# Optimization experiments

Hardware: AMD Instinct MI355X
Metric: run time of the kernel (lower is better)

The kernel has to match this reference:

```python
import jax, jax.numpy as jnp
import numpy as np

N_HEAD = 8
HEAD_DIM = 128
WINDOW = 512
ROPE_BASE = 10000.0


def _rope_tables(T, dtype):
    # inv_freq: [head_dim/2]
    inv_freq = 1.0 / (ROPE_BASE ** (jnp.arange(0, HEAD_DIM, 2, dtype=jnp.float32) / HEAD_DIM))
    t = jnp.arange(T, dtype=jnp.float32)
    freqs = jnp.einsum('i,j->ij', t, inv_freq)          # [T, head_dim/2]
    emb = jnp.concatenate([freqs, freqs], axis=-1)       # [T, head_dim]
    return jnp.cos(emb).astype(dtype), jnp.sin(emb).astype(dtype)


def _rotate_half(x):
    d = x.shape[-1] // 2
    return jnp.concatenate([-x[..., d:], x[..., :d]], axis=-1)


def setup_inputs() -> dict:
    key = jax.random.key(0)
    k1, k2, k3 = jax.random.split(key, 3)
    B, T, C = 2, 4096, 1024
    x = jax.random.normal(k1, (B, T, C), dtype=jnp.float32)
    w_qkv = jax.random.normal(k2, (3 * C, C), dtype=jnp.float32) * (1.0 / np.sqrt(C))
    w_o = jax.random.normal(k3, (C, C), dtype=jnp.float32) * (1.0 / np.sqrt(C))
    return {"x": x, "w_qkv": w_qkv, "w_o": w_o}


def reference(x, w_qkv, w_o):
    B, T, C = x.shape
    scale = 1.0 / np.sqrt(HEAD_DIM)
    qkv = x @ w_qkv.T                                     # [B,T,3C]
    q, k, v = jnp.split(qkv, 3, axis=-1)
    # [B, H, T, D]
    q = q.reshape(B, T, N_HEAD, HEAD_DIM).transpose(0, 2, 1, 3)
    k = k.reshape(B, T, N_HEAD, HEAD_DIM).transpose(0, 2, 1, 3)
    v = v.reshape(B, T, N_HEAD, HEAD_DIM).transpose(0, 2, 1, 3)
    cos, sin = _rope_tables(T, x.dtype)                   # [T, D]
    cos = cos[None, None]
    sin = sin[None, None]
    q = q * cos + _rotate_half(q) * sin
    k = k * cos + _rotate_half(k) * sin
    attn = jnp.einsum('bhqd,bhkd->bhqk', q, k) * scale    # [B,H,T,T]
    i = jnp.arange(T)[:, None]
    j = jnp.arange(T)[None, :]
    # causal (j<=i) AND sliding window triu(diag=-W) (j >= i - W)
    keep = (j <= i) & (j >= i - WINDOW)
    neg = jnp.finfo(attn.dtype).min
    attn = jnp.where(keep[None, None], attn, neg)
    attn = jax.nn.softmax(attn, axis=-1)
    out = jnp.einsum('bhqk,bhkd->bhqd', attn, v)          # [B,H,T,D]
    out = out.transpose(0, 2, 1, 3).reshape(B, T, C)
    return out @ w_o.T
```

## Files before the change

kernel.cpp:

```cpp
#include <hip/hip_runtime.h>
#include <hip/hip_bf16.h>

typedef unsigned short us;
typedef __attribute__((ext_vector_type(8))) __bf16 bf16x8;
typedef __attribute__((ext_vector_type(4))) float f32x4;

#define MFMA16(a, b, c) __builtin_amdgcn_mfma_f32_16x16x32_bf16(a, b, c, 0, 0, 0)

static __device__ __forceinline__ us f2bf(float f) {
  __hip_bfloat16 h = __float2bfloat16(f);
  return __builtin_bit_cast(us, h);
}

static __device__ __forceinline__ void gll16(const us* g, us* l) {
  __builtin_amdgcn_global_load_lds((const __attribute__((address_space(1))) void*)g,
                                   (__attribute__((address_space(3))) void*)l,
                                   16, 0, 0);
}

__global__ void prep_kernel(const float* __restrict__ x, const float* __restrict__ wq,
                            const float* __restrict__ wo, us* __restrict__ xb,
                            us* __restrict__ wqb, us* __restrict__ wob,
                            float* __restrict__ ct, float* __restrict__ st) {
  const int blk = blockIdx.x;
  const int tid = threadIdx.x;
  if (blk < 12288) {
    const float* in;
    us* out;
    int i;
    if (blk < 8192)      { in = x;  out = xb;  i = blk * 256 + tid; }
    else if (blk < 11264){ in = wq; out = wqb; i = (blk - 8192) * 256 + tid; }
    else                 { in = wo; out = wob; i = (blk - 11264) * 256 + tid; }
    float4 v = ((const float4*)in)[i];
    ushort4 o;
    o.x = f2bf(v.x); o.y = f2bf(v.y); o.z = f2bf(v.z); o.w = f2bf(v.w);
    ((ushort4*)out)[i] = o;
  } else {
    int i = (blk - 12288) * 256 + tid;
    int t = i >> 6, d = i & 63;
    float ang = (float)t * exp2f((float)d * -0.20762050593046014f);
    float s, c;
    sincosf(ang, &s, &c);
    ct[i] = c;
    st[i] = s;
  }
}

__global__ __launch_bounds__(256, 2)
void qkv_rope_kernel(const us* __restrict__ A, const us* __restrict__ B,
                     const float* __restrict__ ctab, const float* __restrict__ stab,
                     us* __restrict__ qb, us* __restrict__ kb, us* __restrict__ vtb) {
  __shared__ __align__(16) char smem_raw[128 * 132 * 4];
  us* sA = (us*)smem_raw;
  us* sB = sA + 128 * 64;
  float* sC = (float*)smem_raw;
  us* sCus = (us*)smem_raw;

  const int tid = threadIdx.x;
  const int lane = tid & 63;
  const int wave = tid >> 6;
  const int l15 = lane & 15;
  const int lq = lane >> 4;
  const int m0 = blockIdx.x * 128;
  const int n0 = blockIdx.y * 128;
  const int wm = (wave & 1) * 64;
  const int wn2 = (wave >> 1) * 32;

  f32x4 acc[4][4] = {};

  for (int k0 = 0; k0 < 1024; k0 += 64) {
    for (int i = 0; i < 4; ++i) {
      int c = wave * 4 + i;
      int P = c * 64 + lane;
      int row = P >> 3;
      int cb = (P & 7) ^ (row & 7);
      gll16(A + (size_t)(m0 + row) * 1024 + k0 + cb * 8, sA + c * 512);
      gll16(B + (size_t)(n0 + row) * 1024 + k0 + cb * 8, sB + c * 512);
    }
    __syncthreads();
#pragma unroll
    for (int kk = 0; kk < 64; kk += 32) {
      const int cbr = (kk + lq * 8) >> 3;
      bf16x8 av[4], bv[4];
#pragma unroll
      for (int mt = 0; mt < 4; ++mt) {
        int m = wm + mt * 16 + l15;
        av[mt] = *(const bf16x8*)(sA + (m * 8 + (cbr ^ (m & 7))) * 8);
      }
#pragma unroll
      for (int nt = 0; nt < 4; ++nt) {
        int n = wn2 + (nt & 1) * 16 + (nt >> 1) * 64 + l15;
        bv[nt] = *(const bf16x8*)(sB + (n * 8 + (cbr ^ (n & 7))) * 8);
      }
#pragma unroll
      for (int mt = 0; mt < 4; ++mt)
#pragma unroll
        for (int nt = 0; nt < 4; ++nt)
          acc[mt][nt] = MFMA16(av[mt], bv[nt], acc[mt][nt]);
    }
    __syncthreads();
  }

  const int b = m0 >> 12;
  const int t0 = m0 & 4095;
  const int which = blockIdx.y >> 3;
  const int h = blockIdx.y & 7;

  if (which < 2) {
    us* outp = (which == 0) ? qb : kb;
    const size_t obase = ((size_t)(b * 8 + h)) * 4096 * 128;
#pragma unroll
    for (int mt = 0; mt < 4; ++mt)
#pragma unroll
      for (int r = 0; r < 4; ++r) {
        const int row = wm + mt * 16 + lq * 4 + r;
        const int tg = t0 + row;
        const float* cp = ctab + tg * 64 + wn2 + l15;
        const float* sp = stab + tg * 64 + wn2 + l15;
        const float c0 = cp[0], c1 = cp[16], s0 = sp[0], s1 = sp[16];
#pragma unroll
        for (int nt = 0; nt < 4; ++nt) {
          float xv = acc[mt][nt][r];
          float xp = acc[mt][nt ^ 2][r];
          float rot = (nt < 2) ? -xp : xp;
          float y = xv * ((nt & 1) ? c1 : c0) + rot * ((nt & 1) ? s1 : s0);
          sCus[row * 136 + wn2 + (nt & 1) * 16 + (nt >> 1) * 64 + l15] = f2bf(y);
        }
      }
    __syncthreads();
    for (int r = 0; r < 8; ++r) {
      int row = (tid >> 4) + r * 16;
      int col = (tid & 15) * 8;
      uint4 v = *(const uint4*)(sCus + row * 136 + col);
      *(uint4*)(outp + obase + (size_t)(t0 + row) * 128 + col) = v;
    }
  } else {
#pragma unroll
    for (int mt = 0; mt < 4; ++mt)
#pragma unroll
      for (int nt = 0; nt < 4; ++nt) {
        const int col = wn2 + (nt & 1) * 16 + (nt >> 1) * 64 + l15;
#pragma unroll
        for (int r = 0; r < 4; ++r)
          sC[(wm + mt * 16 + lq * 4 + r) * 129 + col] = acc[mt][nt][r];
      }
    __syncthreads();
    for (int r = 0; r < 8; ++r) {
      int d = (tid >> 4) + r * 16;
      int tl0 = (tid & 15) * 8;
      union { us u[8]; uint4 v; } tmp;
#pragma unroll
      for (int j = 0; j < 8; ++j)
        tmp.u[j] = f2bf(sC[(tl0 + j) * 129 + d]);
      *(uint4*)(vtb + ((size_t)((b * 8 + h) * 128 + d)) * 4096 + t0 + tl0) = tmp.v;
    }
  }
}

template <int MASK>
__device__ __forceinline__ void p_write(f32x4 (&s)[2][4], us* __restrict__ sP,
                                        int t0, int tj0, int wm2, int lq, int l15) {
  const float C2 = 0.08838834764831845f * 1.4426950408889634f;
#pragma unroll
  for (int mt = 0; mt < 2; ++mt)
#pragma unroll
    for (int nt = 0; nt < 4; ++nt) {
      const int jg = tj0 + nt * 16 + l15;
      const int cb = (nt * 16 + l15) >> 3;
      const int co = l15 & 7;
#pragma unroll
      for (int r = 0; r < 4; ++r) {
        const int rowl = wm2 + mt * 16 + lq * 4 + r;
        float v = s[mt][nt][r];
        if (MASK == 1) v = (jg + 512 >= t0 + rowl) ? v : -3.0e38f;
        if (MASK == 2) v = (jg <= t0 + rowl) ? v : -3.0e38f;
        sP[rowl * 64 + ((cb ^ (rowl & 7)) * 8) + co] = f2bf(exp2f(v * C2));
      }
    }
}

__global__ __launch_bounds__(256, 2)
void flash_kernel(const us* __restrict__ qg, const us* __restrict__ kg,
                  const us* __restrict__ vg, us* __restrict__ ao) {
  __shared__ us smem[40960];
  us* sK = smem;
  us* sV = smem + 16384;
  us* sP = smem + 32768;

  const int tid = threadIdx.x;
  const int lane = tid & 63;
  const int wave = tid >> 6;
  const int l15 = lane & 15;
  const int lq = lane >> 4;
  const int qx = blockIdx.x;
  const int h = blockIdx.y;
  const int b = blockIdx.z;
  const int t0 = qx * 128;
  const size_t bh = (size_t)(b * 8 + h);
  const int wm2 = wave * 32;

  bf16x8 qf[2][4];
#pragma unroll
  for (int mt = 0; mt < 2; ++mt)
#pragma unroll
    for (int ks = 0; ks < 4; ++ks)
      qf[mt][ks] = *(const bf16x8*)(qg + (bh * 4096 + t0 + wm2 + mt * 16 + l15) * 128 +
                                    ks * 32 + lq * 8);

  union { us u[8]; bf16x8 v; } one_u;
#pragma unroll
  for (int i = 0; i < 8; ++i) one_u.u[i] = 0x3F80;
  const bf16x8 vone = one_u.v;

  f32x4 o[2][9] = {};

  const int lo = t0 - 512;
  const int jtmin = (lo <= 0) ? 0 : (lo >> 6);
  const int jtmax = (t0 + 127) >> 6;
  const bool wmask = (t0 >= 512);

  auto stage = [&](int jt, int buf) {
    const int tj0 = jt * 64;
    us* dK = sK + buf * 8192;
    us* dV = sV + buf * 8192;
    for (int i = 0; i < 4; ++i) {
      int c = wave * 4 + i;
      int P = c * 64 + lane;
      int rowK = P >> 4;
      int cbK = (P & 15) ^ (rowK & 15);
      gll16(kg + (bh * 4096 + tj0 + rowK) * 128 + cbK * 8, dK + c * 512);
      int rowV = P >> 3;
      int cbV = (P & 7) ^ (rowV & 7);
      gll16(vg + (bh * 128 + rowV) * 4096 + tj0 + cbV * 8, dV + c * 512);
    }
  };

  stage(jtmin, 0);
  int cur = 0;

  for (int jt = jtmin; jt <= jtmax; ++jt) {
    __syncthreads();
    if (jt < jtmax) stage(jt + 1, cur ^ 1);

    const int tj0 = jt * 64;
    const us* sKc = sK + cur * 8192;
    const us* sVc = sV + cur * 8192;

    f32x4 s[2][4] = {};
#pragma unroll
    for (int ks = 0; ks < 4; ++ks) {
      const int cbr = ks * 4 + lq;
#pragma unroll
      for (int nt = 0; nt < 4; ++nt) {
        int n = nt * 16 + l15;
        bf16x8 bk = *(const bf16x8*)(sKc + (n * 16 + (cbr ^ (n & 15))) * 8);
#pragma unroll
        for (int mt = 0; mt < 2; ++mt)
          s[mt][nt] = MFMA16(qf[mt][ks], bk, s[mt][nt]);
      }
    }

    if (jt >= jtmax - 1)               p_write<2>(s, sP, t0, tj0, wm2, lq, l15);
    else if (wmask && jt <= jtmin + 1) p_write<1>(s, sP, t0, tj0, wm2, lq, l15);
    else                               p_write<0>(s, sP, t0, tj0, wm2, lq, l15);

#pragma unroll
    for (int ks = 0; ks < 2; ++ks) {
#pragma unroll
      for (int mt = 0; mt < 2; ++mt) {
        bf16x8 ap = *(const bf16x8*)(sP + (wm2 + mt * 16 + l15) * 64 +
                                     (((ks * 4 + lq) ^ (l15 & 7)) * 8));
#pragma unroll
        for (int dt = 0; dt < 8; ++dt) {
          int dd = dt * 16 + l15;
          bf16x8 bv = *(const bf16x8*)(sVc + (dd * 8 + ((ks * 4 + lq) ^ (dd & 7))) * 8);
          o[mt][dt] = MFMA16(ap, bv, o[mt][dt]);
        }
        o[mt][8] = MFMA16(ap, vone, o[mt][8]);
      }
    }
    cur ^= 1;
  }

#pragma unroll
  for (int mt = 0; mt < 2; ++mt)
#pragma unroll
    for (int r = 0; r < 4; ++r) {
      const float inv = 1.0f / o[mt][8][r];
      const int rowl = wm2 + mt * 16 + lq * 4 + r;
      const size_t base = ((size_t)b * 4096 + t0 + rowl) * 1024 + h * 128;
#pragma unroll
      for (int dt = 0; dt < 8; ++dt)
        ao[base + dt * 16 + l15] = f2bf(o[mt][dt][r] * inv);
    }
}

__global__ __launch_bounds__(256, 2)
void out_proj_kernel(const us* __restrict__ A, const us* __restrict__ B, float* __restrict__ C) {
  __shared__ us sA[128 * 64];
  __shared__ us sB[128 * 64];
  const int tid = threadIdx.x;
  const int lane = tid & 63;
  const int wave = tid >> 6;
  const int l15 = lane & 15;
  const int lq = lane >> 4;
  const int m0 = blockIdx.x * 128;
  const int n0 = blockIdx.y * 128;
  const int wm = (wave & 1) * 64;
  const int wn = (wave >> 1) * 64;
  f32x4 acc[4][4] = {};
  for (int k0 = 0; k0 < 1024; k0 += 64) {
    for (int i = 0; i < 4; ++i) {
      int c = wave * 4 + i;
      int P = c * 64 + lane;
      int row = P >> 3;
      int cb = (P & 7) ^ (row & 7);
      gll16(A + (size_t)(m0 + row) * 1024 + k0 + cb * 8, sA + c * 512);
      gll16(B + (size_t)(n0 + row) * 1024 + k0 + cb * 8, sB + c * 512);
    }
    __syncthreads();
#pragma unroll
    for (int kk = 0; kk < 64; kk += 32) {
      const int cbr = (kk + lq * 8) >> 3;
      bf16x8 av[4], bv[4];
#pragma unroll
      for (int mt = 0; mt < 4; ++mt) {
        int m = wm + mt * 16 + l15;
        av[mt] = *(const bf16x8*)(sA + (m * 8 + (cbr ^ (m & 7))) * 8);
      }
#pragma unroll
      for (int nt = 0; nt < 4; ++nt) {
        int n = wn + nt * 16 + l15;
        bv[nt] = *(const bf16x8*)(sB + (n * 8 + (cbr ^ (n & 7))) * 8);
      }
#pragma unroll
      for (int mt = 0; mt < 4; ++mt)
#pragma unroll
        for (int nt = 0; nt < 4; ++nt)
          acc[mt][nt] = MFMA16(av[mt], bv[nt], acc[mt][nt]);
    }
    __syncthreads();
  }
#pragma unroll
  for (int mt = 0; mt < 4; ++mt)
#pragma unroll
    for (int nt = 0; nt < 4; ++nt)
#pragma unroll
      for (int r = 0; r < 4; ++r)
        C[(size_t)(m0 + wm + mt * 16 + lq * 4 + r) * 1024 + (n0 + wn + nt * 16 + l15)] =
            acc[mt][nt][r];
}

extern "C" void kernel_launch(void* const* d_in, const int* in_sizes, int n_in,
                              void* d_out, int out_size, void* d_ws, size_t ws_size,
                              hipStream_t stream) {
  const float* x     = (const float*)d_in[0];
  const float* w_qkv = (const float*)d_in[1];
  const float* w_o   = (const float*)d_in[2];
  float* out = (float*)d_out;

  us* xb  = (us*)d_ws;
  us* wqb = xb  + (size_t)8192 * 1024;
  us* wob = wqb + (size_t)3072 * 1024;
  us* qb  = wob + (size_t)1024 * 1024;
  us* kb  = qb  + (size_t)2 * 8 * 4096 * 128;
  us* vtb = kb  + (size_t)2 * 8 * 4096 * 128;
  us* aob = vtb + (size_t)2 * 8 * 4096 * 128;
  float* ctab = (float*)(aob + (size_t)8192 * 1024);
  float* stab = ctab + (size_t)4096 * 64;

  prep_kernel<<<13312, 256, 0, stream>>>(x, w_qkv, w_o, xb, wqb, wob, ctab, stab);
  qkv_rope_kernel<<<dim3(64, 24), 256, 0, stream>>>(xb, wqb, ctab, stab, qb, kb, vtb);
  flash_kernel<<<dim3(32, 8, 2), 256, 0, stream>>>(qb, kb, vtb, aob);
  out_proj_kernel<<<dim3(64, 8), 256, 0, stream>>>(aob, wob, out);
}
```

Measured before the change: 208.2 us.

## Rewrite QKV GEMM as 256x256 tile, 8-wave double-buffered pipelined kernel

The QKV projection GEMM moves from 128x128 tiles with 4 waves to 256x256 tiles with 8 waves. LDS is double-buffered and each K-step is split into four quarter phases that interleave LDS fragment reads, asynchronous global-to-LDS prefetch of the next tiles, and MFMA bursts. Raised wave priority and explicit waitcnt and barriers are used to overlap loads with compute. The epilogue now handles two heads per block, with RoPE and the V transpose going through LDS. This gives more reuse per loaded byte and fewer blocks (384), at the cost of more registers, a complex schedule, and possible tail imbalance across CUs.

```diff
diff --git a/kernel.cpp b/kernel.cpp
--- a/kernel.cpp
+++ b/kernel.cpp
@@ -6,6 +6,7 @@
 typedef __attribute__((ext_vector_type(4))) float f32x4;
 
 #define MFMA16(a, b, c) __builtin_amdgcn_mfma_f32_16x16x32_bf16(a, b, c, 0, 0, 0)
+#define FENCE asm volatile("" ::: "memory")
 
 static __device__ __forceinline__ us f2bf(float f) {
   __hip_bfloat16 h = __float2bfloat16(f);
@@ -46,113 +47,210 @@
   }
 }
 
-__global__ __launch_bounds__(256, 2)
+__global__ __launch_bounds__(512, 2)
 void qkv_rope_kernel(const us* __restrict__ A, const us* __restrict__ B,
                      const float* __restrict__ ctab, const float* __restrict__ stab,
                      us* __restrict__ qb, us* __restrict__ kb, us* __restrict__ vtb) {
-  __shared__ __align__(16) char smem_raw[128 * 132 * 4];
-  us* sA = (us*)smem_raw;
-  us* sB = sA + 128 * 64;
-  float* sC = (float*)smem_raw;
-  us* sCus = (us*)smem_raw;
+  __shared__ __align__(16) us smem[65536];
+  us* sAb = smem;
+  us* sBb = smem + 32768;
 
   const int tid = threadIdx.x;
   const int lane = tid & 63;
   const int wave = tid >> 6;
   const int l15 = lane & 15;
   const int lq = lane >> 4;
-  const int m0 = blockIdx.x * 128;
-  const int n0 = blockIdx.y * 128;
-  const int wm = (wave & 1) * 64;
-  const int wn2 = (wave >> 1) * 32;
-
-  f32x4 acc[4][4] = {};
-
-  for (int k0 = 0; k0 < 1024; k0 += 64) {
-    for (int i = 0; i < 4; ++i) {
-      int c = wave * 4 + i;
-      int P = c * 64 + lane;
-      int row = P >> 3;
-      int cb = (P & 7) ^ (row & 7);
-      gll16(A + (size_t)(m0 + row) * 1024 + k0 + cb * 8, sA + c * 512);
-      gll16(B + (size_t)(n0 + row) * 1024 + k0 + cb * 8, sB + c * 512);
-    }
-    __syncthreads();
-#pragma unroll
-    for (int kk = 0; kk < 64; kk += 32) {
-      const int cbr = (kk + lq * 8) >> 3;
-      bf16x8 av[4], bv[4];
-#pragma unroll
-      for (int mt = 0; mt < 4; ++mt) {
-        int m = wm + mt * 16 + l15;
-        av[mt] = *(const bf16x8*)(sA + (m * 8 + (cbr ^ (m & 7))) * 8);
-      }
-#pragma unroll
-      for (int nt = 0; nt < 4; ++nt) {
-        int n = wn2 + (nt & 1) * 16 + (nt >> 1) * 64 + l15;
-        bv[nt] = *(const bf16x8*)(sB + (n * 8 + (cbr ^ (n & 7))) * 8);
-      }
-#pragma unroll
-      for (int mt = 0; mt < 4; ++mt)
-#pragma unroll
-        for (int nt = 0; nt < 4; ++nt)
-          acc[mt][nt] = MFMA16(av[mt], bv[nt], acc[mt][nt]);
-    }
-    __syncthreads();
+  const int wr = wave >> 2;
+  const int wc = wave & 3;
+  const int m0 = blockIdx.x * 256;
+  const int n0 = blockIdx.y * 256;
+
+  auto stage = [&](const us* gbase, us* lds, int j) {
+    int P = j * 512 + tid;
+    int row = P >> 3;
+    int sb = (P & 7) ^ (row & 7);
+    gll16(gbase + (size_t)row * 1024 + sb * 8, lds + (j * 512 + wave * 64) * 8);
+  };
+  auto stage_half = [&](int t, int h) {
+    int c = t & 1;
+    const us* g;
+    us* l;
+    if (h < 2) { g = A + (size_t)(m0 + h * 128) * 1024 + t * 64; l = sAb + c * 16384 + h * 8192; }
+    else       { g = B + (size_t)(n0 + (h - 2) * 128) * 1024 + t * 64; l = sBb + c * 16384 + (h - 2) * 8192; }
+    stage(g, l, 0);
+    stage(g, l, 1);
+  };
+  auto nrow = [&](int nt) {
+    return (wc >> 1) * 128 + (wc & 1) * 32 + (nt & 1) * 16 + (nt >> 1) * 64 + l15;
+  };
+
+  f32x4 acc[8][4] = {};
+  bf16x8 a0[4][2], a1[4][2], b0[2][2], b1[2][2];
+
+#pragma unroll
+  for (int h = 0; h < 4; ++h) stage_half(0, h);
+  stage_half(1, 0); stage_half(1, 1); stage_half(1, 2);
+  asm volatile("s_waitcnt vmcnt(6)" ::: "memory");
+  FENCE; __builtin_amdgcn_s_barrier(); FENCE;
+
+  for (int kt = 0; kt < 16; ++kt) {
+    const int c = kt & 1;
+    const us* sAc = sAb + c * 16384;
+    const us* sBc = sBb + c * 16384;
+
+#pragma unroll
+    for (int mt = 0; mt < 4; ++mt)
+#pragma unroll
+      for (int kk = 0; kk < 2; ++kk) {
+        int m = wr * 128 + mt * 16 + l15;
+        a0[mt][kk] = *(const bf16x8*)(sAc + m * 64 + (((kk * 4 + lq) ^ (m & 7)) * 8));
+      }
+#pragma unroll
+    for (int nt = 0; nt < 2; ++nt)
+#pragma unroll
+      for (int kk = 0; kk < 2; ++kk) {
+        int n = nrow(nt);
+        b0[nt][kk] = *(const bf16x8*)(sBc + n * 64 + (((kk * 4 + lq) ^ (n & 7)) * 8));
+      }
+    if (kt < 15) stage_half(kt + 1, 3);
+    FENCE; __builtin_amdgcn_s_barrier(); FENCE;
+    asm volatile("s_waitcnt lgkmcnt(0)" ::: "memory");
+    __builtin_amdgcn_sched_barrier(0);
+    __builtin_amdgcn_s_setprio(1);
+#pragma unroll
+    for (int mt = 0; mt < 4; ++mt)
+#pragma unroll
+      for (int nt = 0; nt < 2; ++nt)
+#pragma unroll
+        for (int kk = 0; kk < 2; ++kk)
+          acc[mt][nt] = MFMA16(a0[mt][kk], b0[nt][kk], acc[mt][nt]);
+    __builtin_amdgcn_s_setprio(0);
+    FENCE; __builtin_amdgcn_s_barrier(); FENCE;
+
+#pragma unroll
+    for (int mt = 0; mt < 4; ++mt)
+#pragma unroll
+      for (int kk = 0; kk < 2; ++kk) {
+        int m = wr * 128 + 64 + mt * 16 + l15;
+        a1[mt][kk] = *(const bf16x8*)(sAc + m * 64 + (((kk * 4 + lq) ^ (m & 7)) * 8));
+      }
+    FENCE; __builtin_amdgcn_s_barrier(); FENCE;
+    asm volatile("s_waitcnt lgkmcnt(0)" ::: "memory");
+    __builtin_amdgcn_sched_barrier(0);
+    __builtin_amdgcn_s_setprio(1);
+#pragma unroll
+    for (int mt = 0; mt < 4; ++mt)
+#pragma unroll
+      for (int nt = 0; nt < 2; ++nt)
+#pragma unroll
+        for (int kk = 0; kk < 2; ++kk)
+          acc[4 + mt][nt] = MFMA16(a1[mt][kk], b0[nt][kk], acc[4 + mt][nt]);
+    __builtin_amdgcn_s_setprio(0);
+    FENCE; __builtin_amdgcn_s_barrier(); FENCE;
+
+#pragma unroll
+    for (int nt = 0; nt < 2; ++nt)
+#pragma unroll
+      for (int kk = 0; kk < 2; ++kk) {
+        int n = nrow(2 + nt);
+        b1[nt][kk] = *(const bf16x8*)(sBc + n * 64 + (((kk * 4 + lq) ^ (n & 7)) * 8));
+      }
+    if (kt < 14) stage_half(kt + 2, 0);
+    FENCE; __builtin_amdgcn_s_barrier(); FENCE;
+    asm volatile("s_waitcnt lgkmcnt(0)" ::: "memory");
+    __builtin_amdgcn_sched_barrier(0);
+    __builtin_amdgcn_s_setprio(1);
+#pragma unroll
+    for (int mt = 0; mt < 4; ++mt)
+#pragma unroll
+      for (int nt = 0; nt < 2; ++nt)
+#pragma unroll
+        for (int kk = 0; kk < 2; ++kk)
+          acc[4 + mt][2 + nt] = MFMA16(a1[mt][kk], b1[nt][kk], acc[4 + mt][2 + nt]);
+    __builtin_amdgcn_s_setprio(0);
+    FENCE; __builtin_amdgcn_s_barrier(); FENCE;
+
+    if (kt < 14) { stage_half(kt + 2, 1); stage_half(kt + 2, 2); }
+    FENCE; __builtin_amdgcn_s_barrier(); FENCE;
+    __builtin_amdgcn_s_setprio(1);
+#pragma unroll
+    for (int mt = 0; mt < 4; ++mt)
+#pragma unroll
+      for (int nt = 0; nt < 2; ++nt)
+#pragma unroll
+        for (int kk = 0; kk < 2; ++kk)
+          acc[mt][2 + nt] = MFMA16(a0[mt][kk], b1[nt][kk], acc[mt][2 + nt]);
+    __builtin_amdgcn_s_setprio(0);
+    if (kt < 14) { asm volatile("s_waitcnt vmcnt(6)" ::: "memory"); }
+    else         { asm volatile("s_waitcnt vmcnt(0)" ::: "memory"); }
+    FENCE; __builtin_amdgcn_s_barrier(); FENCE;
   }
 
   const int b = m0 >> 12;
-  const int t0 = m0 & 4095;
-  const int which = blockIdx.y >> 3;
-  const int h = blockIdx.y & 7;
+  const int tg0 = m0 & 4095;
+  const int g0 = blockIdx.y * 2;
+  const int which = g0 >> 3;
+  us* sE = smem;
 
   if (which < 2) {
     us* outp = (which == 0) ? qb : kb;
-    const size_t obase = ((size_t)(b * 8 + h)) * 4096 * 128;
-#pragma unroll
-    for (int mt = 0; mt < 4; ++mt)
-#pragma unroll
-      for (int r = 0; r < 4; ++r) {
-        const int row = wm + mt * 16 + lq * 4 + r;
-        const int tg = t0 + row;
-        const float* cp = ctab + tg * 64 + wn2 + l15;
-        const float* sp = stab + tg * 64 + wn2 + l15;
-        const float c0 = cp[0], c1 = cp[16], s0 = sp[0], s1 = sp[16];
-#pragma unroll
-        for (int nt = 0; nt < 4; ++nt) {
-          float xv = acc[mt][nt][r];
-          float xp = acc[mt][nt ^ 2][r];
-          float rot = (nt < 2) ? -xp : xp;
-          float y = xv * ((nt & 1) ? c1 : c0) + rot * ((nt & 1) ? s1 : s0);
-          sCus[row * 136 + wn2 + (nt & 1) * 16 + (nt >> 1) * 64 + l15] = f2bf(y);
-        }
-      }
-    __syncthreads();
-    for (int r = 0; r < 8; ++r) {
-      int row = (tid >> 4) + r * 16;
-      int col = (tid & 15) * 8;
-      uint4 v = *(const uint4*)(sCus + row * 136 + col);
-      *(uint4*)(outp + obase + (size_t)(t0 + row) * 128 + col) = v;
+    for (int ch = 0; ch < 2; ++ch) {
+      const int h = (g0 + ch) & 7;
+      if ((wc >> 1) == ch) {
+        const int dl0 = (wc & 1) * 32 + l15;
+#pragma unroll
+        for (int mt = 0; mt < 8; ++mt)
+#pragma unroll
+          for (int r = 0; r < 4; ++r) {
+            const int row = wr * 128 + mt * 16 + lq * 4 + r;
+            const int tg = tg0 + row;
+            const float c0 = ctab[tg * 64 + dl0], c1 = ctab[tg * 64 + dl0 + 16];
+            const float s0 = stab[tg * 64 + dl0], s1 = stab[tg * 64 + dl0 + 16];
+#pragma unroll
+            for (int nt = 0; nt < 4; ++nt) {
+              float xv = acc[mt][nt][r];
+              float xp = acc[mt][nt ^ 2][r];
+              float rot = (nt < 2) ? -xp : xp;
+              float y = xv * ((nt & 1) ? c1 : c0) + rot * ((nt & 1) ? s1 : s0);
+              sE[row * 136 + (wc & 1) * 32 + (nt & 1) * 16 + (nt >> 1) * 64 + l15] = f2bf(y);
+            }
+          }
+      }
+      __syncthreads();
+      const size_t obase = ((size_t)(b * 8 + h) * 4096 + tg0) * 128;
+      for (int it = 0; it < 8; ++it) {
+        int idx = it * 512 + tid;
+        int row = idx >> 4;
+        int col = (idx & 15) * 8;
+        *(uint4*)(outp + obase + (size_t)row * 128 + col) = *(const uint4*)(sE + row * 136 + col);
+      }
+      __syncthreads();
     }
   } else {
-#pragma unroll
-    for (int mt = 0; mt < 4; ++mt)
-#pragma unroll
-      for (int nt = 0; nt < 4; ++nt) {
-        const int col = wn2 + (nt & 1) * 16 + (nt >> 1) * 64 + l15;
-#pragma unroll
-        for (int r = 0; r < 4; ++r)
-          sC[(wm + mt * 16 + lq * 4 + r) * 129 + col] = acc[mt][nt][r];
-      }
-    __syncthreads();
-    for (int r = 0; r < 8; ++r) {
-      int d = (tid >> 4) + r * 16;
-      int tl0 = (tid & 15) * 8;
-      union { us u[8]; uint4 v; } tmp;
-#pragma unroll
-      for (int j = 0; j < 8; ++j)
-        tmp.u[j] = f2bf(sC[(tl0 + j) * 129 + d]);
-      *(uint4*)(vtb + ((size_t)((b * 8 + h) * 128 + d)) * 4096 + t0 + tl0) = tmp.v;
+    for (int ch = 0; ch < 2; ++ch) {
+      const int h = (g0 + ch) & 7;
+      if ((wc >> 1) == ch) {
+#pragma unroll
+        for (int mt = 0; mt < 8; ++mt)
+#pragma unroll
+          for (int nt = 0; nt < 4; ++nt) {
+            const int dl = (wc & 1) * 32 + (nt & 1) * 16 + (nt >> 1) * 64 + l15;
+#pragma unroll
+            for (int r = 0; r < 4; ++r) {
+              const int row = wr * 128 + mt * 16 + lq * 4 + r;
+              sE[dl * 264 + row] = f2bf(acc[mt][nt][r]);
+            }
+          }
+      }
+      __syncthreads();
+      const size_t obase = (size_t)(b * 8 + h) * 128 * 4096 + tg0;
+      for (int it = 0; it < 8; ++it) {
+        int idx = it * 512 + tid;
+        int d = idx >> 5;
+        int tl = (idx & 31) * 8;
+        *(uint4*)(vtb + obase + (size_t)d * 4096 + tl) = *(const uint4*)(sE + d * 264 + tl);
+      }
+      __syncthreads();
     }
   }
 }
@@ -370,7 +468,7 @@
   float* stab = ctab + (size_t)4096 * 64;
 
   prep_kernel<<<13312, 256, 0, stream>>>(x, w_qkv, w_o, xb, wqb, wob, ctab, stab);
-  qkv_rope_kernel<<<dim3(64, 24), 256, 0, stream>>>(xb, wqb, ctab, stab, qb, kb, vtb);
+  qkv_rope_kernel<<<dim3(32, 12), 512, 0, stream>>>(xb, wqb, ctab, stab, qb, kb, vtb);
   flash_kernel<<<dim3(32, 8, 2), 256, 0, stream>>>(qb, kb, vtb, aob);
   out_proj_kernel<<<dim3(64, 8), 256, 0, stream>>>(aob, wob, out);
 }
```

After: 249.3 us. 19.7% more time.
